# Optimization experiments

Measured on AMD Instinct MI355X. Metric: run time of the kernel, lower is better.

The kernel has to match this reference:

```python
import jax, jax.numpy as jnp
import numpy as np

EPS = 1e-5  # BatchNorm eps


def _unfold3x3(x):
    """torch.nn.Unfold(kernel=3, pad=1, stride=1) -> [B, H*W, 9, C] layout.

    Kernel positions are row-major (kh, kw); index 4 is the center, matching
    x_pn[:, :, 4:5, :] in the torch module.
    """
    B, C, H, W = x.shape
    xp = jnp.pad(x, ((0, 0), (0, 0), (1, 1), (1, 1)))
    patches = jnp.stack([xp[:, :, i:i + H, j:j + W]
                         for i in range(3) for j in range(3)], axis=1)  # [B,9,C,H,W]
    return patches.transpose(0, 3, 4, 1, 2).reshape(B, H * W, 9, C)


def setup_inputs() -> dict:
    key = jax.random.key(0)
    ks = jax.random.split(key, 10)
    B, Cin, Cout, H, W = 2, 64, 64, 64, 2048
    Ctot = 4 + Cin  # 4 meta channels + feature channels
    return {
        "x": jax.random.normal(ks[0], (B, Ctot, H, W), jnp.float32),
        "mask": jax.random.randint(ks[1], (B, 1, H, W), 0, 2, jnp.int32),
        # weight_mlp1: Linear(4 -> Cin, bias=False), torch layout [out, in]
        "W1": jax.random.normal(ks[2], (Cin, 4), jnp.float32) * 0.3,
        "bn1_g": jnp.ones((Cin,), jnp.float32),
        "bn1_b": jnp.zeros((Cin,), jnp.float32),
        "bn1_m": jax.random.normal(ks[3], (Cin,), jnp.float32) * 0.1,
        "bn1_v": jax.random.uniform(ks[4], (Cin,), jnp.float32, 0.5, 1.5),
        # weight_mlp2: Linear(Cin -> 1) (attention head)
        "W2": jax.random.normal(ks[5], (1, Cin), jnp.float32) * 0.1,
        "b2": jnp.zeros((1,), jnp.float32),
        # aggregation_mlp: Linear(9*Cin -> Cout, bias=False)
        "Wagg": jax.random.normal(ks[6], (Cout, 9 * Cin), jnp.float32) * 0.04,
        "bn2_g": jnp.ones((Cout,), jnp.float32),
        "bn2_b": jnp.zeros((Cout,), jnp.float32),
        "bn2_m": jax.random.normal(ks[7], (Cout,), jnp.float32) * 0.1,
        "bn2_v": jax.random.uniform(ks[8], (Cout,), jnp.float32, 0.5, 1.5),
    }


def reference(x, mask, W1, bn1_g, bn1_b, bn1_m, bn1_v, W2, b2,
              Wagg, bn2_g, bn2_b, bn2_m, bn2_v):
    B, Ctot, H, W_ = x.shape
    Cin = W1.shape[0]

    xu = _unfold3x3(x)                       # [B, HW, 9, Ctot]
    feats = xu[..., 4:]                      # [B, HW, 9, Cin]
    pn = xu[..., :4]                         # meta coords of 9 neighbors
    d = pn - pn[:, :, 4:5, :]                # relative to center pixel

    # per-neighbor weight MLP (Linear -> BN(eval) -> ReLU -> Linear)
    w = jnp.einsum('bnkm,cm->bnkc', d, W1)   # [B, HW, 9, Cin]
    w = (w - bn1_m) * (bn1_g * jax.lax.rsqrt(bn1_v + EPS)) + bn1_b
    w = jax.nn.relu(w)
    w = jnp.einsum('bnkc,oc->bnko', w, W2) + b2  # [B, HW, 9, 1]

    mu = _unfold3x3(mask.astype(jnp.float32))    # [B, HW, 9, 1]
    w = w * mu                                   # masked logits
    w = jax.nn.softmax(w[..., 0], axis=-1)[..., None]  # attention over 9 neighbors

    out = (w * feats).reshape(B, H * W_, 9 * Cin)
    y = jnp.einsum('bnf,of->bno', out, Wagg)     # [B, HW, Cout]
    y = (y - bn2_m) * (bn2_g * jax.lax.rsqrt(bn2_v + EPS)) + bn2_b
    y = jax.nn.relu(y)
    # Fold(kernel=1) == reshape back to the feature map
    return y.transpose(0, 2, 1).reshape(B, -1, H, W_)
```

## Files before the change

### kernel.cpp

```cpp
#include <hip/hip_runtime.h>

#define H_ 64
#define W_ 2048
#define HWsz (H_*W_)
#define CIN 64
#define CTOT 68
#define COUT 64

#define XH 66
#define XW 2050

typedef float  f32x4  __attribute__((ext_vector_type(4)));
typedef float  f32x16 __attribute__((ext_vector_type(16)));
typedef short  s16x8  __attribute__((ext_vector_type(8)));

__device__ __forceinline__ unsigned short f2bf(float f) {
    unsigned u = __builtin_bit_cast(unsigned, f);
    unsigned r = u + 0x7fffu + ((u >> 16) & 1u);
    return (unsigned short)(r >> 16);
}

__global__ __launch_bounds__(256) void prep_bw(
    const float* __restrict__ Wagg,
    const float* __restrict__ W1, const float* __restrict__ g1,
    const float* __restrict__ b1, const float* __restrict__ m1,
    const float* __restrict__ v1, const float* __restrict__ W2,
    unsigned short* __restrict__ BwS, float* __restrict__ Wfold)
{
    int tid = threadIdx.x;
    if (blockIdx.x == 0) {
        if (tid < 64) {
            float s1 = g1[tid] * rsqrtf(v1[tid] + 1e-5f);
#pragma unroll
            for (int m = 0; m < 4; ++m) Wfold[tid*8 + m] = W1[tid*4 + m] * s1;
            Wfold[tid*8 + 4] = b1[tid] - m1[tid]*s1;
            Wfold[tid*8 + 5] = W2[tid];
            Wfold[tid*8 + 6] = 0.f;
            Wfold[tid*8 + 7] = 0.f;
        }
        __syncthreads();
        if (tid == 0) {
            float s = 0.f;
            for (int c = 0; c < 64; ++c) s += fmaxf(Wfold[c*8 + 4], 0.f) * Wfold[c*8 + 5];
            Wfold[512] = s;
        }
    }
    int idx = blockIdx.x * 256 + tid;
    if (idx < 4608) {
        int lane = idx & 63;
        int rest = idx >> 6;
        int nt = rest & 1;
        int ks = (rest >> 1) & 3;
        int k9 = rest >> 3;
        int o  = nt*32 + (lane & 31);
        int ch = ks*16 + (lane >> 5)*8;
        const float* src = Wagg + (size_t)o*(9*CIN) + k9*64 + ch;
        s16x8 v8;
#pragma unroll
        for (int j = 0; j < 8; ++j) v8[j] = (short)f2bf(src[j]);
        *(s16x8*)(BwS + (size_t)idx*8) = v8;
    }
}

__global__ __launch_bounds__(256) void prep_xpm(
    const float* __restrict__ x, const int* __restrict__ mask,
    unsigned short* __restrict__ xpad,
    float* __restrict__ pospad, float* __restrict__ maskpad)
{
    int wc = blockIdx.x * 256 + threadIdx.x;
    if (wc >= XW) return;
    int hr = blockIdx.y;
    int b  = blockIdx.z;
    bool interior = (hr >= 1) && (hr <= H_) && (wc >= 1) && (wc <= W_);
    const float* srcf = x + ((size_t)b*CTOT + 4)*HWsz + (size_t)(hr-1)*W_ + (wc-1);
    unsigned short* dst0 = xpad + ((((size_t)b*XH + hr)*8)*XW + wc)*8;
#pragma unroll
    for (int g = 0; g < 8; ++g) {
        s16x8 v8 = {0,0,0,0,0,0,0,0};
        if (interior) {
            const float* s = srcf + (size_t)(g*8)*HWsz;
#pragma unroll
            for (int j = 0; j < 8; ++j) v8[j] = (short)f2bf(s[(size_t)j*HWsz]);
        }
        *(s16x8*)(dst0 + (size_t)g*XW*8) = v8;
    }
    const float* srcp = x + (size_t)b*CTOT*HWsz + (size_t)(hr-1)*W_ + (wc-1);
#pragma unroll
    for (int ch = 0; ch < 4; ++ch) {
        float v = interior ? srcp[(size_t)ch*HWsz] : 0.f;
        pospad[(((size_t)b*XH + hr)*4 + ch)*XW + wc] = v;
    }
    float mv = interior ? (float)mask[((size_t)b*H_ + (hr-1))*W_ + (wc-1)] : 0.f;
    maskpad[((size_t)b*XH + hr)*XW + wc] = mv;
}

__global__ __launch_bounds__(256, 5) void fused_k(
    const unsigned short* __restrict__ xpad,
    const float* __restrict__ pospad, const float* __restrict__ maskpad,
    const unsigned short* __restrict__ BwS, const float* __restrict__ Wfold,
    const float* __restrict__ b2p,
    const float* __restrict__ g2, const float* __restrict__ bb2,
    const float* __restrict__ m2, const float* __restrict__ v2,
    float* __restrict__ out)
{
    __shared__ __align__(16) unsigned short fe[3][8][66][8];
    __shared__ __align__(16) float sw[9][64];
    __shared__ __align__(16) float sbn[2][64];

    int tid = threadIdx.x;
    int bx = blockIdx.x, by = blockIdx.y;
    int b = by >> 6, h = by & 63;
    int w0 = bx << 6;
    int lane = tid & 63, wv = tid >> 6;

    const unsigned short* xb = xpad + (size_t)b*XH*8*XW*8;

#pragma unroll
    for (int it = 0; it < 6; ++it) {
        int u = it*4 + wv;
        int g = u & 7, r = u >> 3;
        const unsigned short* gsrc = xb + ((((size_t)(h + r)*8 + g)*XW) + w0 + 1 + lane)*8;
        unsigned short* ldst = &fe[r][g][1][0];
        __builtin_amdgcn_global_load_lds(
            (const __attribute__((address_space(1))) unsigned int*)gsrc,
            (__attribute__((address_space(3))) unsigned int*)ldst, 16, 0, 0);
    }
    s16x8 haloV = {0,0,0,0,0,0,0,0};
    int hg = 0, hr3 = 0, hc2 = 0;
    if (tid < 48) {
        hc2 = tid & 1; hg = (tid >> 1) & 7; hr3 = tid >> 4;
        haloV = *(const s16x8*)(xb + ((((size_t)(h + hr3)*8 + hg)*XW) + w0 + hc2*65)*8);
    }
    if (tid >= 192) {
        int o = tid - 192;
        float sc = g2[o] * rsqrtf(v2[o] + 1e-5f);
        sbn[0][o] = sc;
        sbn[1][o] = bb2[o] - m2[o]*sc;
    }

    int px = tid & 63, grp = wv;
    int k0 = 2*grp + (grp >> 1);
    int k1 = k0 + 1;
    const float* pb = pospad + (size_t)b*XH*4*XW;
    const float* mb = maskpad + (size_t)b*XH*XW;
    int gw = w0 + px;

    float pc[4], dd[2][4], mu[2];
#pragma unroll
    for (int ch = 0; ch < 4; ++ch)
        pc[ch] = pb[((size_t)(h+1)*4 + ch)*XW + gw + 1];
    {
        int r0 = k0/3, d0 = k0%3, r1 = k1/3, d1 = k1%3;
#pragma unroll
        for (int ch = 0; ch < 4; ++ch) {
            dd[0][ch] = pb[((size_t)(h+r0)*4 + ch)*XW + gw + d0] - pc[ch];
            dd[1][ch] = pb[((size_t)(h+r1)*4 + ch)*XW + gw + d1] - pc[ch];
        }
        mu[0] = mb[(size_t)(h+r0)*XW + gw + d0];
        mu[1] = mb[(size_t)(h+r1)*XW + gw + d1];
    }

    float lg[2] = {0.f, 0.f};
    const f32x4* Wf4 = (const f32x4*)Wfold;
#pragma unroll 8
    for (int c = 0; c < CIN; ++c) {
        f32x4 wa = Wf4[2*c];
        f32x4 wb = Wf4[2*c + 1];
#pragma unroll
        for (int t = 0; t < 2; ++t) {
            float v = fmaf(dd[t][0], wa[0], fmaf(dd[t][1], wa[1],
                      fmaf(dd[t][2], wa[2], fmaf(dd[t][3], wa[3], wb[0]))));
            lg[t] += fmaxf(v, 0.f) * wb[1];
        }
    }
    float b2v = b2p[0];
    sw[k0][px] = (lg[0] + b2v) * mu[0];
    sw[k1][px] = (lg[1] + b2v) * mu[1];
    if (tid < 48) *(s16x8*)&fe[hr3][hg][hc2*65][0] = haloV;
    __syncthreads();

    if (tid < 64) {
        float mu4 = mb[(size_t)(h+1)*XW + w0 + tid + 1];
        float lgv[9];
#pragma unroll
        for (int k = 0; k < 9; ++k) if (k != 4) lgv[k] = sw[k][tid];
        lgv[4] = (Wfold[512] + b2v) * mu4;
        float mx = -1e30f;
#pragma unroll
        for (int k = 0; k < 9; ++k) mx = fmaxf(mx, lgv[k]);
        float s = 0.f, e[9];
#pragma unroll
        for (int k = 0; k < 9; ++k) { e[k] = __expf(lgv[k] - mx); s += e[k]; }
        float inv = 1.f / s;
#pragma unroll
        for (int k = 0; k < 9; ++k) sw[k][tid] = e[k] * inv;
    }
    __syncthreads();

    int nt = wv & 1, mh = wv >> 1;
    int l31 = lane & 31, l5 = lane >> 5;

    const f32x16 fz16 = {0.f,0.f,0.f,0.f,0.f,0.f,0.f,0.f,0.f,0.f,0.f,0.f,0.f,0.f,0.f,0.f};
    f32x16 fin = fz16;

#pragma unroll
    for (int k9 = 0; k9 < 9; ++k9) {
        const int r = k9/3, dwp = k9%3;
        int col = mh*32 + l31 + dwp;

        s16x8 aw[4];
#pragma unroll
        for (int ks = 0; ks < 4; ++ks)
            aw[ks] = *(const s16x8*)(BwS + (size_t)((((k9<<2) + ks)*2 + nt) << 9) + lane*8);

        f32x16 tmp = fz16;
#pragma unroll
        for (int ks = 0; ks < 4; ++ks) {
            s16x8 bfr = *(const s16x8*)&fe[r][ks*2 + l5][col][0];
            tmp = __builtin_amdgcn_mfma_f32_32x32x16_bf16(aw[ks], bfr, tmp, 0, 0, 0);
        }
        float wsc = sw[k9][mh*32 + l31];
#pragma unroll
        for (int c = 0; c < 16; ++c) fin[c] += wsc * tmp[c];
    }

    int obase = nt*32 + 4*l5;
    float* od = out + (((size_t)b*COUT + obase)*H_ + h)*W_ + w0 + mh*32 + l31;
#pragma unroll
    for (int v = 0; v < 4; ++v) {
        f32x4 sc4 = *(const f32x4*)&sbn[0][obase + 8*v];
        f32x4 tc4 = *(const f32x4*)&sbn[1][obase + 8*v];
#pragma unroll
        for (int c = 0; c < 4; ++c) {
            float val = fmaxf(fmaf(fin[4*v + c], sc4[c], tc4[c]), 0.f);
            od[(size_t)(8*v + c)*HWsz] = val;
        }
    }
}

extern "C" void kernel_launch(void* const* d_in, const int* in_sizes, int n_in,
                              void* d_out, int out_size, void* d_ws, size_t ws_size,
                              hipStream_t stream)
{
    const float* x    = (const float*)d_in[0];
    const int*   mask = (const int*)d_in[1];
    const float* W1   = (const float*)d_in[2];
    const float* g1   = (const float*)d_in[3];
    const float* b1   = (const float*)d_in[4];
    const float* m1   = (const float*)d_in[5];
    const float* v1   = (const float*)d_in[6];
    const float* W2   = (const float*)d_in[7];
    const float* b2   = (const float*)d_in[8];
    const float* Wagg = (const float*)d_in[9];
    const float* g2   = (const float*)d_in[10];
    const float* bb2  = (const float*)d_in[11];
    const float* m2   = (const float*)d_in[12];
    const float* v2   = (const float*)d_in[13];
    float* outp = (float*)d_out;

    char* ws = (char*)d_ws;
    unsigned short* xpad    = (unsigned short*)(ws + 0);
    float*          pospad  = (float*)(ws + 34636800);
    float*          maskpad = (float*)(ws + 38966400);
    unsigned short* BwS     = (unsigned short*)(ws + 40048800);
    float*          Wfold   = (float*)(ws + 40122528);

    hipLaunchKernelGGL(prep_bw, dim3(18), dim3(256), 0, stream,
                       Wagg, W1, g1, b1, m1, v1, W2, BwS, Wfold);
    hipLaunchKernelGGL(prep_xpm, dim3((XW + 255)/256, XH, 2), dim3(256), 0, stream,
                       x, mask, xpad, pospad, maskpad);
    hipLaunchKernelGGL(fused_k, dim3(W_/64, 128), dim3(256), 0, stream,
                       xpad, pospad, maskpad, BwS, Wfold, b2,
                       g2, bb2, m2, v2, outp);
}
```

Baseline: 202.4 us.

## Fuse input padding/bf16 conversion into main kernel and process two rows per block

Removes the separate prep pass that wrote padded bf16 features, position and mask buffers. The main kernel now reads fp32 x and the int mask directly, converts to bf16 into LDS with bounds checks, and handles two output rows per block so the 4-row halo is shared. The weight MLP is also vectorised over pairs of taps. This cuts a full read/write round trip of the input through the workspace, at the cost of uncoalesced strided fp32 loads in the main kernel and lower occupancy (launch bound 4 instead of 5).

```diff
diff --git a/kernel.cpp b/kernel.cpp
--- a/kernel.cpp
+++ b/kernel.cpp
@@ -1,4 +1,5 @@
 #include <hip/hip_runtime.h>
+#include <hip/hip_bf16.h>
 
 #define H_ 64
 #define W_ 2048
@@ -7,9 +8,7 @@
 #define CTOT 68
 #define COUT 64
 
-#define XH 66
-#define XW 2050
-
+typedef float  f32x2  __attribute__((ext_vector_type(2)));
 typedef float  f32x4  __attribute__((ext_vector_type(4)));
 typedef float  f32x16 __attribute__((ext_vector_type(16)));
 typedef short  s16x8  __attribute__((ext_vector_type(8)));
@@ -18,6 +17,13 @@
     unsigned u = __builtin_bit_cast(unsigned, f);
     unsigned r = u + 0x7fffu + ((u >> 16) & 1u);
     return (unsigned short)(r >> 16);
+}
+
+__device__ __forceinline__ unsigned pack2bf(float a, float b) {
+    __hip_bfloat162 h = __float22bfloat162_rn(float2{a, b});
+    unsigned u;
+    __builtin_memcpy(&u, &h, 4);
+    return u;
 }
 
 __global__ __launch_bounds__(256) void prep_bw(
@@ -62,75 +68,52 @@
     }
 }
 
-__global__ __launch_bounds__(256) void prep_xpm(
+template<int KB>
+__device__ __forceinline__ void tap_load(
+    const float* __restrict__ xp, const int* __restrict__ mk,
+    int h, int gw, const float pc[4], f32x2 dd2[2][4], f32x2 mu2[2])
+{
+#pragma unroll
+    for (int i = 0; i < 4; ++i) {
+        const int k = KB + i;
+        const int r = k/3 - 1, d = k%3 - 1;
+        int ih = h + r, iw = gw + d;
+        bool ok = ((unsigned)ih < (unsigned)H_) && ((unsigned)iw < (unsigned)W_);
+        int ihc = min(max(ih, 0), H_-1);
+        int iwc = min(max(iw, 0), W_-1);
+        float m = ok ? (float)mk[(size_t)ihc*W_ + iwc] : 0.f;
+        mu2[i>>1][i&1] = m;
+#pragma unroll
+        for (int ch = 0; ch < 4; ++ch) {
+            float p = xp[(size_t)ch*HWsz + (size_t)ihc*W_ + iwc];
+            p = ok ? p : 0.f;
+            dd2[i>>1][ch][i&1] = p - pc[ch];
+        }
+    }
+}
+
+__global__ __launch_bounds__(256, 4) void mega_k(
     const float* __restrict__ x, const int* __restrict__ mask,
-    unsigned short* __restrict__ xpad,
-    float* __restrict__ pospad, float* __restrict__ maskpad)
-{
-    int wc = blockIdx.x * 256 + threadIdx.x;
-    if (wc >= XW) return;
-    int hr = blockIdx.y;
-    int b  = blockIdx.z;
-    bool interior = (hr >= 1) && (hr <= H_) && (wc >= 1) && (wc <= W_);
-    const float* srcf = x + ((size_t)b*CTOT + 4)*HWsz + (size_t)(hr-1)*W_ + (wc-1);
-    unsigned short* dst0 = xpad + ((((size_t)b*XH + hr)*8)*XW + wc)*8;
-#pragma unroll
-    for (int g = 0; g < 8; ++g) {
-        s16x8 v8 = {0,0,0,0,0,0,0,0};
-        if (interior) {
-            const float* s = srcf + (size_t)(g*8)*HWsz;
-#pragma unroll
-            for (int j = 0; j < 8; ++j) v8[j] = (short)f2bf(s[(size_t)j*HWsz]);
-        }
-        *(s16x8*)(dst0 + (size_t)g*XW*8) = v8;
-    }
-    const float* srcp = x + (size_t)b*CTOT*HWsz + (size_t)(hr-1)*W_ + (wc-1);
-#pragma unroll
-    for (int ch = 0; ch < 4; ++ch) {
-        float v = interior ? srcp[(size_t)ch*HWsz] : 0.f;
-        pospad[(((size_t)b*XH + hr)*4 + ch)*XW + wc] = v;
-    }
-    float mv = interior ? (float)mask[((size_t)b*H_ + (hr-1))*W_ + (wc-1)] : 0.f;
-    maskpad[((size_t)b*XH + hr)*XW + wc] = mv;
-}
-
-__global__ __launch_bounds__(256, 5) void fused_k(
-    const unsigned short* __restrict__ xpad,
-    const float* __restrict__ pospad, const float* __restrict__ maskpad,
     const unsigned short* __restrict__ BwS, const float* __restrict__ Wfold,
     const float* __restrict__ b2p,
     const float* __restrict__ g2, const float* __restrict__ bb2,
     const float* __restrict__ m2, const float* __restrict__ v2,
     float* __restrict__ out)
 {
-    __shared__ __align__(16) unsigned short fe[3][8][66][8];
-    __shared__ __align__(16) float sw[9][64];
+    __shared__ __align__(16) unsigned short fe[4][8][66][8];
+    __shared__ __align__(16) float sw[2][9][64];
     __shared__ __align__(16) float sbn[2][64];
 
-    int tid = threadIdx.x;
-    int bx = blockIdx.x, by = blockIdx.y;
-    int b = by >> 6, h = by & 63;
-    int w0 = bx << 6;
-    int lane = tid & 63, wv = tid >> 6;
-
-    const unsigned short* xb = xpad + (size_t)b*XH*8*XW*8;
-
-#pragma unroll
-    for (int it = 0; it < 6; ++it) {
-        int u = it*4 + wv;
-        int g = u & 7, r = u >> 3;
-        const unsigned short* gsrc = xb + ((((size_t)(h + r)*8 + g)*XW) + w0 + 1 + lane)*8;
-        unsigned short* ldst = &fe[r][g][1][0];
-        __builtin_amdgcn_global_load_lds(
-            (const __attribute__((address_space(1))) unsigned int*)gsrc,
-            (__attribute__((address_space(3))) unsigned int*)ldst, 16, 0, 0);
-    }
-    s16x8 haloV = {0,0,0,0,0,0,0,0};
-    int hg = 0, hr3 = 0, hc2 = 0;
-    if (tid < 48) {
-        hc2 = tid & 1; hg = (tid >> 1) & 7; hr3 = tid >> 4;
-        haloV = *(const s16x8*)(xb + ((((size_t)(h + hr3)*8 + hg)*XW) + w0 + hc2*65)*8);
-    }
+    const int tid = threadIdx.x;
+    const int bx = blockIdx.x, by = blockIdx.y;
+    const int b = by >> 5, h0 = (by & 31) << 1;
+    const int w0 = bx << 6;
+    const int lane = tid & 63, wv = tid >> 6;
+
+    const float* xf = x + ((size_t)b*CTOT + 4)*HWsz;
+    const float* xp = x + (size_t)b*CTOT*HWsz;
+    const int*   mk = mask + (size_t)b*HWsz;
+
     if (tid >= 192) {
         int o = tid - 192;
         float sc = g2[o] * rsqrtf(v2[o] + 1e-5f);
@@ -138,52 +121,81 @@
         sbn[1][o] = bb2[o] - m2[o]*sc;
     }
 
-    int px = tid & 63, grp = wv;
-    int k0 = 2*grp + (grp >> 1);
-    int k1 = k0 + 1;
-    const float* pb = pospad + (size_t)b*XH*4*XW;
-    const float* mb = maskpad + (size_t)b*XH*XW;
-    int gw = w0 + px;
-
-    float pc[4], dd[2][4], mu[2];
-#pragma unroll
-    for (int ch = 0; ch < 4; ++ch)
-        pc[ch] = pb[((size_t)(h+1)*4 + ch)*XW + gw + 1];
-    {
-        int r0 = k0/3, d0 = k0%3, r1 = k1/3, d1 = k1%3;
-#pragma unroll
-        for (int ch = 0; ch < 4; ++ch) {
-            dd[0][ch] = pb[((size_t)(h+r0)*4 + ch)*XW + gw + d0] - pc[ch];
-            dd[1][ch] = pb[((size_t)(h+r1)*4 + ch)*XW + gw + d1] - pc[ch];
-        }
-        mu[0] = mb[(size_t)(h+r0)*XW + gw + d0];
-        mu[1] = mb[(size_t)(h+r1)*XW + gw + d1];
-    }
-
-    float lg[2] = {0.f, 0.f};
+#pragma unroll
+    for (int it = 0; it < 8; ++it) {
+        int u = it*4 + wv;
+        int g = u & 7, r = u >> 3;
+        int gr = h0 - 1 + r;
+        uint4 q = {0u, 0u, 0u, 0u};
+        if ((unsigned)gr < (unsigned)H_) {
+            const float* src = xf + (size_t)(g*8)*HWsz + (size_t)gr*W_ + w0 + lane;
+            float v[8];
+#pragma unroll
+            for (int j = 0; j < 8; ++j) v[j] = src[(size_t)j*HWsz];
+            q.x = pack2bf(v[0], v[1]); q.y = pack2bf(v[2], v[3]);
+            q.z = pack2bf(v[4], v[5]); q.w = pack2bf(v[6], v[7]);
+        }
+        *(uint4*)&fe[r][g][1 + lane][0] = q;
+    }
+    if (tid < 64) {
+        int c2 = tid & 1, g = (tid >> 1) & 7, r = tid >> 4;
+        int gr = h0 - 1 + r, gc = w0 - 1 + c2*65;
+        uint4 q = {0u, 0u, 0u, 0u};
+        if (((unsigned)gr < (unsigned)H_) && ((unsigned)gc < (unsigned)W_)) {
+            const float* src = xf + (size_t)(g*8)*HWsz + (size_t)gr*W_ + gc;
+            float v[8];
+#pragma unroll
+            for (int j = 0; j < 8; ++j) v[j] = src[(size_t)j*HWsz];
+            q.x = pack2bf(v[0], v[1]); q.y = pack2bf(v[2], v[3]);
+            q.z = pack2bf(v[4], v[5]); q.w = pack2bf(v[6], v[7]);
+        }
+        *(uint4*)&fe[r][g][c2*65][0] = q;
+    }
+
+    const int px = tid & 63, gw = w0 + px;
+    const int rowq = wv >> 1, tg = wv & 1;
+    const int h = h0 + rowq;
+
+    float pc[4];
+#pragma unroll
+    for (int ch = 0; ch < 4; ++ch) pc[ch] = xp[(size_t)ch*HWsz + (size_t)h*W_ + gw];
+
+    f32x2 dd2[2][4]; f32x2 mu2[2];
+    if (tg == 0) tap_load<0>(xp, mk, h, gw, pc, dd2, mu2);
+    else         tap_load<5>(xp, mk, h, gw, pc, dd2, mu2);
+
     const f32x4* Wf4 = (const f32x4*)Wfold;
+    const f32x2 z2 = {0.f, 0.f};
+    f32x2 lg2[2] = {z2, z2};
 #pragma unroll 8
     for (int c = 0; c < CIN; ++c) {
         f32x4 wa = Wf4[2*c];
         f32x4 wb = Wf4[2*c + 1];
 #pragma unroll
-        for (int t = 0; t < 2; ++t) {
-            float v = fmaf(dd[t][0], wa[0], fmaf(dd[t][1], wa[1],
-                      fmaf(dd[t][2], wa[2], fmaf(dd[t][3], wa[3], wb[0]))));
-            lg[t] += fmaxf(v, 0.f) * wb[1];
+        for (int p = 0; p < 2; ++p) {
+            f32x2 v = {wb[0], wb[0]};
+            v = dd2[p][0]*wa[0] + v;
+            v = dd2[p][1]*wa[1] + v;
+            v = dd2[p][2]*wa[2] + v;
+            v = dd2[p][3]*wa[3] + v;
+            v = __builtin_elementwise_max(v, z2);
+            lg2[p] = v*wb[1] + lg2[p];
         }
     }
     float b2v = b2p[0];
-    sw[k0][px] = (lg[0] + b2v) * mu[0];
-    sw[k1][px] = (lg[1] + b2v) * mu[1];
-    if (tid < 48) *(s16x8*)&fe[hr3][hg][hc2*65][0] = haloV;
+#pragma unroll
+    for (int i = 0; i < 4; ++i) {
+        int k = i + 5*tg;
+        sw[rowq][k][px] = (lg2[i>>1][i&1] + b2v) * mu2[i>>1][i&1];
+    }
     __syncthreads();
 
-    if (tid < 64) {
-        float mu4 = mb[(size_t)(h+1)*XW + w0 + tid + 1];
+    if (tid < 128) {
+        int rq = tid >> 6, p2 = tid & 63;
+        float mu4 = (float)mk[(size_t)(h0 + rq)*W_ + w0 + p2];
         float lgv[9];
 #pragma unroll
-        for (int k = 0; k < 9; ++k) if (k != 4) lgv[k] = sw[k][tid];
+        for (int k = 0; k < 9; ++k) if (k != 4) lgv[k] = sw[rq][k][p2];
         lgv[4] = (Wfold[512] + b2v) * mu4;
         float mx = -1e30f;
 #pragma unroll
@@ -193,47 +205,54 @@
         for (int k = 0; k < 9; ++k) { e[k] = __expf(lgv[k] - mx); s += e[k]; }
         float inv = 1.f / s;
 #pragma unroll
-        for (int k = 0; k < 9; ++k) sw[k][tid] = e[k] * inv;
+        for (int k = 0; k < 9; ++k) sw[rq][k][p2] = e[k] * inv;
     }
     __syncthreads();
 
-    int nt = wv & 1, mh = wv >> 1;
-    int l31 = lane & 31, l5 = lane >> 5;
+    const int nt = wv & 1, rh = wv >> 1;
+    const int l31 = lane & 31, l5 = lane >> 5;
+    const int hC = h0 + rh;
 
     const f32x16 fz16 = {0.f,0.f,0.f,0.f,0.f,0.f,0.f,0.f,0.f,0.f,0.f,0.f,0.f,0.f,0.f,0.f};
-    f32x16 fin = fz16;
+    f32x16 fin[2] = {fz16, fz16};
 
 #pragma unroll
     for (int k9 = 0; k9 < 9; ++k9) {
-        const int r = k9/3, dwp = k9%3;
-        int col = mh*32 + l31 + dwp;
+        const int rr = rh + k9/3;
+        const int dwp = k9 % 3;
 
         s16x8 aw[4];
 #pragma unroll
         for (int ks = 0; ks < 4; ++ks)
             aw[ks] = *(const s16x8*)(BwS + (size_t)((((k9<<2) + ks)*2 + nt) << 9) + lane*8);
 
-        f32x16 tmp = fz16;
-#pragma unroll
-        for (int ks = 0; ks < 4; ++ks) {
-            s16x8 bfr = *(const s16x8*)&fe[r][ks*2 + l5][col][0];
-            tmp = __builtin_amdgcn_mfma_f32_32x32x16_bf16(aw[ks], bfr, tmp, 0, 0, 0);
-        }
-        float wsc = sw[k9][mh*32 + l31];
-#pragma unroll
-        for (int c = 0; c < 16; ++c) fin[c] += wsc * tmp[c];
+#pragma unroll
+        for (int half = 0; half < 2; ++half) {
+            int col = half*32 + l31 + dwp;
+            f32x16 tmp = fz16;
+#pragma unroll
+            for (int ks = 0; ks < 4; ++ks) {
+                s16x8 bfr = *(const s16x8*)&fe[rr][ks*2 + l5][col][0];
+                tmp = __builtin_amdgcn_mfma_f32_32x32x16_bf16(aw[ks], bfr, tmp, 0, 0, 0);
+            }
+            float wsc = sw[rh][k9][half*32 + l31];
+#pragma unroll
+            for (int c = 0; c < 16; ++c) fin[half][c] += wsc * tmp[c];
+        }
     }
 
     int obase = nt*32 + 4*l5;
-    float* od = out + (((size_t)b*COUT + obase)*H_ + h)*W_ + w0 + mh*32 + l31;
-#pragma unroll
-    for (int v = 0; v < 4; ++v) {
-        f32x4 sc4 = *(const f32x4*)&sbn[0][obase + 8*v];
-        f32x4 tc4 = *(const f32x4*)&sbn[1][obase + 8*v];
-#pragma unroll
-        for (int c = 0; c < 4; ++c) {
-            float val = fmaxf(fmaf(fin[4*v + c], sc4[c], tc4[c]), 0.f);
-            od[(size_t)(8*v + c)*HWsz] = val;
+#pragma unroll
+    for (int half = 0; half < 2; ++half) {
+        float* od = out + (((size_t)b*COUT + obase)*H_ + hC)*W_ + w0 + half*32 + l31;
+#pragma unroll
+        for (int v = 0; v < 4; ++v) {
+            f32x4 sc4 = *(const f32x4*)&sbn[0][obase + 8*v];
+            f32x4 tc4 = *(const f32x4*)&sbn[1][obase + 8*v];
+#pragma unroll
+            for (int c = 0; c < 4; ++c)
+                od[(size_t)(8*v + c)*HWsz] =
+                    fmaxf(fmaf(fin[half][4*v + c], sc4[c], tc4[c]), 0.f);
         }
     }
 }
@@ -259,17 +278,11 @@
     float* outp = (float*)d_out;
 
     char* ws = (char*)d_ws;
-    unsigned short* xpad    = (unsigned short*)(ws + 0);
-    float*          pospad  = (float*)(ws + 34636800);
-    float*          maskpad = (float*)(ws + 38966400);
-    unsigned short* BwS     = (unsigned short*)(ws + 40048800);
-    float*          Wfold   = (float*)(ws + 40122528);
+    unsigned short* BwS   = (unsigned short*)(ws + 0);
+    float*          Wfold = (float*)(ws + 73728);
 
     hipLaunchKernelGGL(prep_bw, dim3(18), dim3(256), 0, stream,
                        Wagg, W1, g1, b1, m1, v1, W2, BwS, Wfold);
-    hipLaunchKernelGGL(prep_xpm, dim3((XW + 255)/256, XH, 2), dim3(256), 0, stream,
-                       x, mask, xpad, pospad, maskpad);
-    hipLaunchKernelGGL(fused_k, dim3(W_/64, 128), dim3(256), 0, stream,
-                       xpad, pospad, maskpad, BwS, Wfold, b2,
-                       g2, bb2, m2, v2, outp);
-}
+    hipLaunchKernelGGL(mega_k, dim3(W_/64, 64), dim3(256), 0, stream,
+                       x, mask, BwS, Wfold, b2, g2, bb2, m2, v2, outp);
+}
```

Result: faster. 186.1 us (-8.1%).
